# Kernel optimization log

Measured on AMD Instinct MI355X. Metric: run time of the kernel, lower is better.

The kernel has to match this reference:

```python
import math
import jax, jax.numpy as jnp
import numpy as np

B, S, D, H = 2, 2048, 1024, 16
DH = D // H
DFF = 4 * D
EPS = 1e-6
MASKED_BIAS = -10000.0


def _gelu(x):
    # GPT-2 tanh-approx GELU
    return 0.5 * x * (1.0 + jnp.tanh(math.sqrt(2.0 / math.pi) * (x + 0.044715 * x ** 3)))


def _layernorm(x, w, b):
    mean = jnp.mean(x, axis=-1, keepdims=True)
    var = jnp.mean((x - mean) ** 2, axis=-1, keepdims=True)
    return w * ((x - mean) / jnp.sqrt(var + EPS)) + b


def setup_inputs() -> dict:
    key = jax.random.key(0)
    ks = jax.random.split(key, 6)
    std = 0.02
    return {
        "hidden_states": jax.random.normal(ks[0], (B, S, D), jnp.float32),
        "w_attn": jax.random.normal(ks[1], (D, 3 * D), jnp.float32) * std,
        "b_attn": jnp.zeros((3 * D,), jnp.float32),
        "w_proj": jax.random.normal(ks[2], (D, D), jnp.float32) * std,
        "b_proj": jnp.zeros((D,), jnp.float32),
        "w_fc": jax.random.normal(ks[3], (D, DFF), jnp.float32) * std,
        "b_fc": jnp.zeros((DFF,), jnp.float32),
        "w_fc_proj": jax.random.normal(ks[4], (DFF, D), jnp.float32) * std,
        "b_fc_proj": jnp.zeros((D,), jnp.float32),
        "ln1_w": jnp.ones((D,), jnp.float32),
        "ln1_b": jnp.zeros((D,), jnp.float32),
        "ln2_w": jnp.ones((D,), jnp.float32),
        "ln2_b": jnp.zeros((D,), jnp.float32),
    }


def reference(hidden_states, w_attn, b_attn, w_proj, b_proj, w_fc, b_fc,
              w_fc_proj, b_fc_proj, ln1_w, ln1_b, ln2_w, ln2_b):
    residual = hidden_states
    x = _layernorm(hidden_states, ln1_w, ln1_b)

    # c_attn: [B,S,D] @ [D,3D] + b -> split into q,k,v
    qkv = x @ w_attn + b_attn
    q, k, v = jnp.split(qkv, 3, axis=-1)
    # split heads -> [B,H,S,DH]
    q = q.reshape(B, S, H, DH).transpose(0, 2, 1, 3)
    k = k.reshape(B, S, H, DH).transpose(0, 2, 1, 3)
    v = v.reshape(B, S, H, DH).transpose(0, 2, 1, 3)

    scores = jnp.einsum('bhqd,bhkd->bhqk', q, k) / jnp.sqrt(jnp.float32(DH))
    causal = jnp.tril(jnp.ones((S, S), bool))  # [S,S]
    scores = jnp.where(causal[None, None], scores, jnp.float32(MASKED_BIAS))
    attn = jax.nn.softmax(scores, axis=-1)
    out = jnp.einsum('bhqk,bhkd->bhqd', attn, v)
    out = out.transpose(0, 2, 1, 3).reshape(B, S, D)
    out = out @ w_proj + b_proj

    h = residual + out
    residual = h
    y = _layernorm(h, ln2_w, ln2_b)
    y = _gelu(y @ w_fc + b_fc)
    y = y @ w_fc_proj + b_fc_proj
    return residual + y
```

## Files before the change

kernel.cpp:

```cpp
#include <hip/hip_runtime.h>
#include <cstdint>
#include <cstddef>

typedef unsigned short u16;
typedef float  floatx4 __attribute__((ext_vector_type(4)));
typedef short  short8  __attribute__((ext_vector_type(8)));
typedef u16    usx4    __attribute__((ext_vector_type(4)));
typedef u16    usx8    __attribute__((ext_vector_type(8)));
typedef unsigned uintx2 __attribute__((ext_vector_type(2)));

__device__ __forceinline__ u16 f2b(float f) {
  unsigned u = __float_as_uint(f);
  unsigned r = u + 0x7fffu + ((u >> 16) & 1u);
  return (u16)(r >> 16);
}
__device__ __forceinline__ float b2f(u16 s) {
  return __uint_as_float(((unsigned)s) << 16);
}

__device__ __forceinline__ float gelu_f(float x) {
  const float k = 2.3022082f;
  float u = x * (1.0f + 0.044715f * x * x);
  float t = __builtin_amdgcn_exp2f(-k * u);
  return x * __builtin_amdgcn_rcpf(1.0f + t);
}

__device__ __forceinline__ void gl2lds16(const u16* g, u16* l) {
  __builtin_amdgcn_global_load_lds(
      (const __attribute__((address_space(1))) unsigned int*)g,
      (__attribute__((address_space(3))) unsigned int*)l, 16, 0, 0);
}

#define C2SCALE 0.18033688011112042f

__global__ __launch_bounds__(256) void ln_bf16_kernel(
    const float* __restrict__ in, const float* __restrict__ w,
    const float* __restrict__ b, u16* __restrict__ out)
{
  const int row = blockIdx.x;
  const int t = threadIdx.x;
  const float* p = in + (size_t)row * 1024 + t * 4;
  floatx4 v = *(const floatx4*)p;
  float s  = v.x + v.y + v.z + v.w;
  float ss = v.x*v.x + v.y*v.y + v.z*v.z + v.w*v.w;
  #pragma unroll
  for (int m = 1; m < 64; m <<= 1) {
    s  += __shfl_xor(s,  m);
    ss += __shfl_xor(ss, m);
  }
  __shared__ float red[8];
  if ((t & 63) == 0) { red[(t >> 6)*2] = s; red[(t >> 6)*2 + 1] = ss; }
  __syncthreads();
  s  = red[0] + red[2] + red[4] + red[6];
  ss = red[1] + red[3] + red[5] + red[7];
  const float mean = s * (1.0f / 1024.0f);
  const float var  = ss * (1.0f / 1024.0f) - mean * mean;
  const float rstd = rsqrtf(var + 1e-6f);
  floatx4 wv = *(const floatx4*)(w + t * 4);
  floatx4 bv = *(const floatx4*)(b + t * 4);
  usx4 o = { f2b(wv.x * ((v.x - mean) * rstd) + bv.x),
             f2b(wv.y * ((v.y - mean) * rstd) + bv.y),
             f2b(wv.z * ((v.z - mean) * rstd) + bv.z),
             f2b(wv.w * ((v.w - mean) * rstd) + bv.w) };
  *(usx4*)(out + (size_t)row * 1024 + t * 4) = o;
}

__global__ __launch_bounds__(256) void combine_ln_kernel(
    const u16* __restrict__ p0, const u16* __restrict__ p1,
    const float* __restrict__ res, const float* __restrict__ bias,
    const float* __restrict__ w, const float* __restrict__ b,
    float* __restrict__ hout, u16* __restrict__ yout)
{
  const int row = blockIdx.x;
  const int t = threadIdx.x;
  const size_t i0 = (size_t)row * 1024 + t * 4;
  floatx4 rv = *(const floatx4*)(res + i0);
  usx4 a = *(const usx4*)(p0 + i0);
  usx4 c = *(const usx4*)(p1 + i0);
  floatx4 biasv = *(const floatx4*)(bias + t * 4);
  floatx4 v;
  #pragma unroll
  for (int i = 0; i < 4; ++i) v[i] = rv[i] + b2f(a[i]) + b2f(c[i]) + biasv[i];
  *(floatx4*)(hout + i0) = v;

  float s  = v.x + v.y + v.z + v.w;
  float ss = v.x*v.x + v.y*v.y + v.z*v.z + v.w*v.w;
  #pragma unroll
  for (int m = 1; m < 64; m <<= 1) {
    s  += __shfl_xor(s,  m);
    ss += __shfl_xor(ss, m);
  }
  __shared__ float red[8];
  if ((t & 63) == 0) { red[(t >> 6)*2] = s; red[(t >> 6)*2 + 1] = ss; }
  __syncthreads();
  s  = red[0] + red[2] + red[4] + red[6];
  ss = red[1] + red[3] + red[5] + red[7];
  const float mean = s * (1.0f / 1024.0f);
  const float var  = ss * (1.0f / 1024.0f) - mean * mean;
  const float rstd = rsqrtf(var + 1e-6f);
  floatx4 wv = *(const floatx4*)(w + t * 4);
  floatx4 bv = *(const floatx4*)(b + t * 4);
  usx4 o = { f2b(wv.x * ((v.x - mean) * rstd) + bv.x),
             f2b(wv.y * ((v.y - mean) * rstd) + bv.y),
             f2b(wv.z * ((v.z - mean) * rstd) + bv.z),
             f2b(wv.w * ((v.w - mean) * rstd) + bv.w) };
  *(usx4*)(yout + i0) = o;
}

__device__ __forceinline__ void wtrans_body(
    const float* __restrict__ in, u16* __restrict__ out, int K, int N,
    int bx, int by, int tx, int ty)
{
  __shared__ u16 tile[32][33];
  const int n0 = bx * 32, k0 = by * 32;
  #pragma unroll
  for (int i = 0; i < 4; ++i)
    tile[ty + i*8][tx] = f2b(in[(size_t)(k0 + ty + i*8) * N + n0 + tx]);
  __syncthreads();
  #pragma unroll
  for (int i = 0; i < 4; ++i)
    out[(size_t)(n0 + ty + i*8) * K + k0 + tx] = tile[tx][ty + i*8];
}

__global__ __launch_bounds__(256) void wtrans4_kernel(
    const float* __restrict__ w0, const float* __restrict__ w1,
    const float* __restrict__ w2, const float* __restrict__ w3,
    u16* __restrict__ o0, u16* __restrict__ o1,
    u16* __restrict__ o2, u16* __restrict__ o3)
{
  int blk = blockIdx.x;
  const int tx = threadIdx.x & 31, ty = threadIdx.x >> 5;
  if (blk < 3072) {
    wtrans_body(w0, o0, 1024, 3072, blk % 96, blk / 96, tx, ty);
  } else if (blk < 4096) {
    blk -= 3072; wtrans_body(w1, o1, 1024, 1024, blk % 32, blk / 32, tx, ty);
  } else if (blk < 8192) {
    blk -= 4096; wtrans_body(w2, o2, 1024, 4096, blk % 128, blk / 128, tx, ty);
  } else {
    blk -= 8192; wtrans_body(w3, o3, 4096, 1024, blk % 32, blk / 32, tx, ty);
  }
}

template<int BM, int BN, int FLAGS, int MINW,
         int NX, int NY, int NZ, int RX, int RY, int RZ>
__global__ __launch_bounds__(256, MINW) void gemm_mfma_kernel(
    const u16* __restrict__ A, const u16* __restrict__ Bt,
    const float* __restrict__ bias, const float* __restrict__ Res,
    void* __restrict__ Cout, int M, int N, int K, int kLen, size_t zStride)
{
  constexpr int WM = BM / 2, WN = BN / 2;
  constexpr int MT = WM / 16, NT = WN / 16;
  constexpr int GX = NX / RX, GY = NY / RY, GZ = NZ / RZ;
  __shared__ u16 As[BM * 32];
  __shared__ u16 Bs[BN * 32];

  const int lin = blockIdx.x + NX * (blockIdx.y + NY * blockIdx.z);
  const int xcd = lin & 7;
  const int idx = lin >> 3;
  const int rx = xcd % RX, ry = (xcd / RX) % RY, rz = xcd / (RX * RY);
  const int bx = rx * GX + idx % GX;
  const int by = ry * GY + (idx / GX) % GY;
  const int bz = rz * GZ + idx / (GX * GY);

  const int t = threadIdx.x;
  const int wave = t >> 6, lane = t & 63;
  const int quad = lane >> 4, l16 = lane & 15;
  const int wm = wave >> 1, wn = wave & 1;
  const int bm0 = by * BM, bn0 = bx * BN;
  const int kStart = bz * kLen;

  const int sRow = lane >> 2;
  const int sq   = (lane & 3) ^ ((lane >> 4) & 3);

  const u16* aG[BM / 64];
  u16* aL[BM / 64];
  #pragma unroll
  for (int j = 0; j < BM / 64; ++j) {
    const int band = j * 4 + wave;
    aG[j] = A + (size_t)(bm0 + band * 16 + sRow) * K + kStart + sq * 8;
    aL[j] = As + band * 512;
  }
  const u16* bG[BN / 64];
  u16* bL[BN / 64];
  #pragma unroll
  for (int j = 0; j < BN / 64; ++j) {
    const int band = j * 4 + wave;
    bG[j] = Bt + (size_t)(bn0 + band * 16 + sRow) * K + kStart + sq * 8;
    bL[j] = Bs + band * 512;
  }

  floatx4 acc[MT][NT] = {};
  const int rcol = (quad ^ (l16 >> 2)) << 3;

  for (int k0 = 0; k0 < kLen; k0 += 32) {
    __syncthreads();
    #pragma unroll
    for (int j = 0; j < BM / 64; ++j) gl2lds16(aG[j] + k0, aL[j]);
    #pragma unroll
    for (int j = 0; j < BN / 64; ++j) gl2lds16(bG[j] + k0, bL[j]);
    __syncthreads();

    short8 af[MT], bf[NT];
    #pragma unroll
    for (int mt = 0; mt < MT; ++mt)
      af[mt] = *(const short8*)&As[(wm*WM + mt*16 + l16) * 32 + rcol];
    #pragma unroll
    for (int nt = 0; nt < NT; ++nt)
      bf[nt] = *(const short8*)&Bs[(wn*WN + nt*16 + l16) * 32 + rcol];
    #pragma unroll
    for (int mt = 0; mt < MT; ++mt)
      #pragma unroll
      for (int nt = 0; nt < NT; ++nt)
        acc[mt][nt] = __builtin_amdgcn_mfma_f32_16x16x32_bf16(af[mt], bf[nt], acc[mt][nt], 0, 0, 0);
  }

  const int orow0 = bm0 + wm * WM;
  const int ocol0 = bn0 + wn * WN;
  const size_t zoff = (size_t)bz * zStride;
  #pragma unroll
  for (int nt = 0; nt < NT; ++nt) {
    const int col = ocol0 + nt*16 + l16;
    const float bv = bias ? bias[col] : 0.0f;
    const float postscale = ((FLAGS & 8) && col < 1024) ? C2SCALE : 1.0f;
    #pragma unroll
    for (int mt = 0; mt < MT; ++mt) {
      #pragma unroll
      for (int r = 0; r < 4; ++r) {
        const int row = orow0 + mt*16 + quad*4 + r;
        float v = acc[mt][nt][r] + bv;
        if (FLAGS & 1) v = gelu_f(v);
        if (FLAGS & 8) v *= postscale;
        if (FLAGS & 2) v += Res[(size_t)row * N + col];
        if (FLAGS & 4) ((u16*)Cout)[zoff + (size_t)row * N + col] = f2b(v);
        else           ((float*)Cout)[zoff + (size_t)row * N + col] = v;
      }
    }
  }
}

__global__ __launch_bounds__(256, 4) void attn_mfma_kernel(
    const u16* __restrict__ qkv, u16* __restrict__ opart, float* __restrict__ ml)
{
  __shared__ u16 Ks[64][72];
  __shared__ u16 Vt[64][72];
  __shared__ u16 Ps[64][72];

  const int t    = threadIdx.x;
  const int wave = t >> 6;
  const int lane = t & 63;
  const int quad = lane >> 4;
  const int l16  = lane & 15;
  const int pair = blockIdx.x >> 1;
  const int half = blockIdx.x & 1;
  const int h    = blockIdx.y;
  const int b    = blockIdx.z;

  const size_t base = (size_t)b * 2048 * 3072;
  const int qoff = h * 64;
  const int koff = 1024 + h * 64;
  const int voff = 2048 + h * 64;

  const int prow = t >> 2;
  const int scol = (t & 3) * 16;
  const int kmap = ((prow & 15) << 2) | (prow >> 4);
  const int kpair  = t & 31;
  const int vchunk = t >> 5;

  const size_t obase  = ((((size_t)half * 2 + b) * 16 + h) * 2048) * 64;
  const size_t mlbase = ((((size_t)half * 2 + b) * 16 + h) * 2048) * 2;

  short8 onesb;
  {
    const short v = (l16 == 0) ? (short)0x3F80 : (short)0;
    #pragma unroll
    for (int i = 0; i < 8; ++i) onesb[i] = v;
  }

  #pragma unroll 1
  for (int iter = 0; iter < 2; ++iter) {
    const int qi = iter ? (31 - pair) : pair;
    const int q0 = qi << 6;
    const int T  = qi + 1;
    const int mid = (T + 1) >> 1;
    const int t0 = half ? mid : 0;
    const int t1 = half ? T : mid;

    floatx4 of[4] = {};
    floatx4 ofl = {};
    float m[4];
    #pragma unroll
    for (int r = 0; r < 4; ++r) m[r] = -1e30f;

    if (t0 < t1) {
      __syncthreads();
      {
        const u16* qp = qkv + base + (size_t)(q0 + prow) * 3072 + qoff + scol;
        *(usx8*)&Ks[prow][scol]     = *(const usx8*)qp;
        *(usx8*)&Ks[prow][scol + 8] = *(const usx8*)(qp + 8);
      }
      __syncthreads();
      const short8 qf0 = *(const short8*)&Ks[wave*16 + l16][quad*8];
      const short8 qf1 = *(const short8*)&Ks[wave*16 + l16][32 + quad*8];

      usx8 kr0, kr1, vr0, vr1;
      {
        const int k0 = t0 << 6;
        const u16* kp = qkv + base + (size_t)(k0 + kmap) * 3072 + koff + scol;
        kr0 = *(const usx8*)kp; kr1 = *(const usx8*)(kp + 8);
        const u16* vp = qkv + base + (size_t)(k0 + 2*kpair) * 3072 + voff + vchunk*8;
        vr0 = *(const usx8*)vp; vr1 = *(const usx8*)(vp + 3072);
      }

      for (int tIdx = t0; tIdx < t1; ++tIdx) {
        __syncthreads();
        *(usx8*)&Ks[prow][scol]     = kr0;
        *(usx8*)&Ks[prow][scol + 8] = kr1;
        #pragma unroll
        for (int i = 0; i < 8; ++i)
          *(unsigned*)&Vt[vchunk*8 + i][2*kpair] =
              (unsigned)vr0[i] | ((unsigned)vr1[i] << 16);
        __syncthreads();

        if (tIdx + 1 < t1) {
          const int kn = (tIdx + 1) << 6;
          const u16* kp = qkv + base + (size_t)(kn + kmap) * 3072 + koff + scol;
          kr0 = *(const usx8*)kp; kr1 = *(const usx8*)(kp + 8);
          const u16* vp = qkv + base + (size_t)(kn + 2*kpair) * 3072 + voff + vchunk*8;
          vr0 = *(const usx8*)vp; vr1 = *(const usx8*)(vp + 3072);
        }

        const int k0 = tIdx << 6;
        floatx4 sf[4];
        #pragma unroll
        for (int kt = 0; kt < 4; ++kt) {
          short8 kf0 = *(const short8*)&Ks[kt*16 + l16][quad*8];
          short8 kf1 = *(const short8*)&Ks[kt*16 + l16][32 + quad*8];
          floatx4 z = {};
          z      = __builtin_amdgcn_mfma_f32_16x16x32_bf16(qf0, kf0, z, 0, 0, 0);
          sf[kt] = __builtin_amdgcn_mfma_f32_16x16x32_bf16(qf1, kf1, z, 0, 0, 0);
        }

        const bool diag = (tIdx == qi);
        #pragma unroll
        for (int r = 0; r < 4; ++r) {
          float sv0 = sf[0][r], sv1 = sf[1][r], sv2 = sf[2][r], sv3 = sf[3][r];
          if (diag) {
            const int qrow = q0 + wave*16 + quad*4 + r;
            const int kbase = k0 + 4*l16;
            if (kbase     > qrow) sv0 = -1e30f;
            if (kbase + 1 > qrow) sv1 = -1e30f;
            if (kbase + 2 > qrow) sv2 = -1e30f;
            if (kbase + 3 > qrow) sv3 = -1e30f;
          }
          float mx = fmaxf(fmaxf(sv0, sv1), fmaxf(sv2, sv3));
          #pragma unroll
          for (int msk = 1; msk < 16; msk <<= 1) mx = fmaxf(mx, __shfl_xor(mx, msk, 16));
          const float nm = fmaxf(m[r], mx);
          const float alpha = __builtin_amdgcn_exp2f(m[r] - nm);
          m[r] = nm;
          const unsigned e0 = f2b(__builtin_amdgcn_exp2f(sv0 - nm));
          const unsigned e1 = f2b(__builtin_amdgcn_exp2f(sv1 - nm));
          const unsigned e2 = f2b(__builtin_amdgcn_exp2f(sv2 - nm));
          const unsigned e3 = f2b(__builtin_amdgcn_exp2f(sv3 - nm));
          uintx2 pw = { e0 | (e1 << 16), e2 | (e3 << 16) };
          *(uintx2*)&Ps[wave*16 + quad*4 + r][l16 * 4] = pw;
          #pragma unroll
          for (int dht = 0; dht < 4; ++dht) of[dht][r] *= alpha;
          ofl[r] *= alpha;
        }

        short8 pf0 = *(const short8*)&Ps[wave*16 + l16][quad*8];
        short8 pf1 = *(const short8*)&Ps[wave*16 + l16][32 + quad*8];
        #pragma unroll
        for (int dht = 0; dht < 4; ++dht) {
          short8 vf0 = *(const short8*)&Vt[dht*16 + l16][quad*8];
          short8 vf1 = *(const short8*)&Vt[dht*16 + l16][32 + quad*8];
          of[dht] = __builtin_amdgcn_mfma_f32_16x16x32_bf16(pf0, vf0, of[dht], 0, 0, 0);
          of[dht] = __builtin_amdgcn_mfma_f32_16x16x32_bf16(pf1, vf1, of[dht], 0, 0, 0);
        }
        ofl = __builtin_amdgcn_mfma_f32_16x16x32_bf16(pf0, onesb, ofl, 0, 0, 0);
        ofl = __builtin_amdgcn_mfma_f32_16x16x32_bf16(pf1, onesb, ofl, 0, 0, 0);
      }
    }

    #pragma unroll
    for (int r = 0; r < 4; ++r) {
      const int s = q0 + wave*16 + quad*4 + r;
      u16* orow = opart + obase + (size_t)s * 64;
      #pragma unroll
      for (int dht = 0; dht < 4; ++dht) orow[dht*16 + l16] = f2b(of[dht][r]);
      const float lr = __shfl(ofl[r], quad * 16);
      if (l16 == 0) { ml[mlbase + 2*s] = m[r]; ml[mlbase + 2*s + 1] = lr; }
    }
  }
}

__global__ __launch_bounds__(256) void attn_combine_kernel(
    const u16* __restrict__ opart, const float* __restrict__ ml,
    u16* __restrict__ out)
{
  const int t = threadIdx.x;
  const int s = blockIdx.x * 4 + (t >> 6);
  const int lane = t & 63;
  const int h = blockIdx.y, b = blockIdx.z;

  const size_t o0  = ((((size_t)0 * 2 + b) * 16 + h) * 2048 + s) * 64 + lane;
  const size_t o1  = ((((size_t)1 * 2 + b) * 16 + h) * 2048 + s) * 64 + lane;
  const size_t ml0 = ((((size_t)0 * 2 + b) * 16 + h) * 2048 + s) * 2;
  const size_t ml1 = ((((size_t)1 * 2 + b) * 16 + h) * 2048 + s) * 2;

  const float m0 = ml[ml0], l0 = ml[ml0 + 1];
  const float m1 = ml[ml1], l1 = ml[ml1 + 1];
  const float M  = fmaxf(m0, m1);
  const float w0 = __builtin_amdgcn_exp2f(m0 - M);
  const float w1 = __builtin_amdgcn_exp2f(m1 - M);
  const float L  = w0 * l0 + w1 * l1;
  const float o  = w0 * b2f(opart[o0]) + w1 * b2f(opart[o1]);
  out[((size_t)b * 2048 + s) * 1024 + h * 64 + lane] = f2b(o / L);
}

__global__ __launch_bounds__(256) void ksplit_combine_kernel(
    const u16* __restrict__ p0, const u16* __restrict__ p1,
    const float* __restrict__ res, const float* __restrict__ bias,
    float* __restrict__ out)
{
  const size_t i0 = ((size_t)blockIdx.x * 256 + threadIdx.x) * 8;
  usx8 a = *(const usx8*)(p0 + i0);
  usx8 c = *(const usx8*)(p1 + i0);
  const int col = (int)(i0 & 1023);
  floatx4 bv0 = *(const floatx4*)(bias + col);
  floatx4 bv1 = *(const floatx4*)(bias + col + 4);
  floatx4 h0 = *(const floatx4*)(res + i0);
  floatx4 h1 = *(const floatx4*)(res + i0 + 4);
  floatx4 o0, o1;
  #pragma unroll
  for (int i = 0; i < 4; ++i) o0[i] = h0[i] + b2f(a[i])   + b2f(c[i])   + bv0[i];
  #pragma unroll
  for (int i = 0; i < 4; ++i) o1[i] = h1[i] + b2f(a[4+i]) + b2f(c[4+i]) + bv1[i];
  *(floatx4*)(out + i0)     = o0;
  *(floatx4*)(out + i0 + 4) = o1;
}

extern "C" void kernel_launch(void* const* d_in, const int* in_sizes, int n_in,
                              void* d_out, int out_size, void* d_ws, size_t ws_size,
                              hipStream_t stream) {
  const float* hidden    = (const float*)d_in[0];
  const float* w_attn    = (const float*)d_in[1];
  const float* b_attn    = (const float*)d_in[2];
  const float* w_proj    = (const float*)d_in[3];
  const float* b_proj    = (const float*)d_in[4];
  const float* w_fc      = (const float*)d_in[5];
  const float* b_fc      = (const float*)d_in[6];
  const float* w_fc_proj = (const float*)d_in[7];
  const float* b_fc_proj = (const float*)d_in[8];
  const float* ln1_w     = (const float*)d_in[9];
  const float* ln1_b     = (const float*)d_in[10];
  const float* ln2_w     = (const float*)d_in[11];
  const float* ln2_b     = (const float*)d_in[12];

  char* wsb = (char*)d_ws;
  u16*   qkvb  = (u16*)  (wsb + (size_t)( 0u << 20));
  u16*   xb    = (u16*)  (wsb + (size_t)(24u << 20));
  u16*   opart = (u16*)  (wsb + (size_t)(24u << 20));
  float* mlbuf = (float*)(wsb + (size_t)(40u << 20));
  u16*   attnb = (u16*)  (wsb + (size_t)(42u << 20));
  u16*   wqT   = (u16*)  (wsb + (size_t)(50u << 20));
  u16*   wpT   = (u16*)  (wsb + (size_t)(56u << 20));
  u16*   wfT   = (u16*)  (wsb + (size_t)(58u << 20));
  u16*   wfpT  = (u16*)  (wsb + (size_t)(66u << 20));
  u16*   pproj = (u16*)  (wsb + (size_t)(24u << 20));
  float* hbuf  = (float*)(wsb + (size_t)(42u << 20));
  u16*   yb    = (u16*)  (wsb + (size_t)( 0u << 20));
  u16*   fcb   = (u16*)  (wsb + (size_t)( 8u << 20));
  u16*   pfcp0 = (u16*)  (wsb + (size_t)( 0u << 20));
  u16*   pfcp1 = (u16*)  (wsb + (size_t)(58u << 20));
  const size_t zstr_fcp = ((size_t)58u << 20) / 2;

  wtrans4_kernel<<<dim3(12288), 256, 0, stream>>>(
      w_attn, w_proj, w_fc, w_fc_proj, wqT, wpT, wfT, wfpT);

  ln_bf16_kernel<<<4096, 256, 0, stream>>>(hidden, ln1_w, ln1_b, xb);
  gemm_mfma_kernel<128,128,12,4, 24,32,1, 2,4,1><<<dim3(24, 32, 1), 256, 0, stream>>>(
      xb, wqT, b_attn, nullptr, qkvb, 4096, 3072, 1024, 1024, 0);
  attn_mfma_kernel<<<dim3(32, 16, 2), 256, 0, stream>>>(qkvb, opart, mlbuf);
  attn_combine_kernel<<<dim3(512, 16, 2), 256, 0, stream>>>(opart, mlbuf, attnb);
  gemm_mfma_kernel<128,64,4,4, 16,32,2, 1,4,2><<<dim3(16, 32, 2), 256, 0, stream>>>(
      attnb, wpT, nullptr, nullptr, pproj, 4096, 1024, 1024, 512, 4194304);
  combine_ln_kernel<<<4096, 256, 0, stream>>>(
      pproj, pproj + 4194304, hidden, b_proj, ln2_w, ln2_b, hbuf, yb);
  gemm_mfma_kernel<128,128,5,4, 32,32,1, 2,4,1><<<dim3(32, 32, 1), 256, 0, stream>>>(
      yb, wfT, b_fc, nullptr, fcb, 4096, 4096, 1024, 1024, 0);
  gemm_mfma_kernel<128,64,4,4, 16,32,2, 1,4,2><<<dim3(16, 32, 2), 256, 0, stream>>>(
      fcb, wfpT, nullptr, nullptr, pfcp0, 4096, 1024, 4096, 2048, zstr_fcp);
  ksplit_combine_kernel<<<dim3(2048), 256, 0, stream>>>(
      pfcp0, pfcp1, hbuf, b_fc_proj, (float*)d_out);
}
```

Before: 356.3 us.

## Double-buffer GEMM LDS tiles and use DPP row-max and packed bf16 conversion

The GEMM main loop now keeps two LDS buffers and issues the global-to-LDS loads for the next K slice before computing the current one, so load latency overlaps with MFMA work. In the attention kernel, the 16-lane max reduction uses DPP row operations instead of shuffles, and the manual bf16 rounding is replaced by the hardware v_cvt_pk_bf16_f32 instruction. The cost is doubled LDS use per GEMM block, which may lower occupancy. The unrolled-by-two loop also assumes kLen is a multiple of 64.

Measured after the change: 352.3 us. No clear change (-1.1%).

```diff
diff --git a/kernel.cpp b/kernel.cpp
--- a/kernel.cpp
+++ b/kernel.cpp
@@ -16,6 +16,25 @@
 }
 __device__ __forceinline__ float b2f(u16 s) {
   return __uint_as_float(((unsigned)s) << 16);
+}
+
+__device__ __forceinline__ unsigned cvt_pk_bf16(float lo, float hi) {
+  unsigned r;
+  asm("v_cvt_pk_bf16_f32 %0, %1, %2" : "=v"(r) : "v"(lo), "v"(hi));
+  return r;
+}
+
+__device__ __forceinline__ float rowmax16(float x) {
+  int xi = __float_as_int(x), y;
+  y = __builtin_amdgcn_update_dpp(xi, xi, 0xB1, 0xF, 0xF, false);
+  x = fmaxf(x, __int_as_float(y)); xi = __float_as_int(x);
+  y = __builtin_amdgcn_update_dpp(xi, xi, 0x4E, 0xF, 0xF, false);
+  x = fmaxf(x, __int_as_float(y)); xi = __float_as_int(x);
+  y = __builtin_amdgcn_update_dpp(xi, xi, 0x141, 0xF, 0xF, false);
+  x = fmaxf(x, __int_as_float(y)); xi = __float_as_int(x);
+  y = __builtin_amdgcn_update_dpp(xi, xi, 0x140, 0xF, 0xF, false);
+  x = fmaxf(x, __int_as_float(y));
+  return x;
 }
 
 __device__ __forceinline__ float gelu_f(float x) {
@@ -151,8 +170,8 @@
   constexpr int WM = BM / 2, WN = BN / 2;
   constexpr int MT = WM / 16, NT = WN / 16;
   constexpr int GX = NX / RX, GY = NY / RY, GZ = NZ / RZ;
-  __shared__ u16 As[BM * 32];
-  __shared__ u16 Bs[BN * 32];
+  __shared__ u16 As[2 * BM * 32];
+  __shared__ u16 Bs[2 * BN * 32];
 
   const int lin = blockIdx.x + NX * (blockIdx.y + NY * blockIdx.z);
   const int xcd = lin & 7;
@@ -192,26 +211,35 @@
   floatx4 acc[MT][NT] = {};
   const int rcol = (quad ^ (l16 >> 2)) << 3;
 
-  for (int k0 = 0; k0 < kLen; k0 += 32) {
-    __syncthreads();
-    #pragma unroll
-    for (int j = 0; j < BM / 64; ++j) gl2lds16(aG[j] + k0, aL[j]);
-    #pragma unroll
-    for (int j = 0; j < BN / 64; ++j) gl2lds16(bG[j] + k0, bL[j]);
-    __syncthreads();
-
+  auto stage = [&](int koff, int buf) {
+    #pragma unroll
+    for (int j = 0; j < BM / 64; ++j) gl2lds16(aG[j] + koff, aL[j] + buf * (BM * 32));
+    #pragma unroll
+    for (int j = 0; j < BN / 64; ++j) gl2lds16(bG[j] + koff, bL[j] + buf * (BN * 32));
+  };
+  auto compute = [&](const u16* Asc, const u16* Bsc) {
     short8 af[MT], bf[NT];
     #pragma unroll
     for (int mt = 0; mt < MT; ++mt)
-      af[mt] = *(const short8*)&As[(wm*WM + mt*16 + l16) * 32 + rcol];
+      af[mt] = *(const short8*)&Asc[(wm*WM + mt*16 + l16) * 32 + rcol];
     #pragma unroll
     for (int nt = 0; nt < NT; ++nt)
-      bf[nt] = *(const short8*)&Bs[(wn*WN + nt*16 + l16) * 32 + rcol];
+      bf[nt] = *(const short8*)&Bsc[(wn*WN + nt*16 + l16) * 32 + rcol];
     #pragma unroll
     for (int mt = 0; mt < MT; ++mt)
       #pragma unroll
       for (int nt = 0; nt < NT; ++nt)
         acc[mt][nt] = __builtin_amdgcn_mfma_f32_16x16x32_bf16(af[mt], bf[nt], acc[mt][nt], 0, 0, 0);
+  };
+
+  stage(0, 0);
+  for (int k0 = 0; k0 < kLen; k0 += 64) {
+    __syncthreads();
+    stage(k0 + 32, 1);
+    compute(As, Bs);
+    __syncthreads();
+    if (k0 + 64 < kLen) stage(k0 + 64, 0);
+    compute(As + BM * 32, Bs + BN * 32);
   }
 
   const int orow0 = bm0 + wm * WM;
@@ -353,16 +381,15 @@
             if (kbase + 3 > qrow) sv3 = -1e30f;
           }
           float mx = fmaxf(fmaxf(sv0, sv1), fmaxf(sv2, sv3));
-          #pragma unroll
-          for (int msk = 1; msk < 16; msk <<= 1) mx = fmaxf(mx, __shfl_xor(mx, msk, 16));
+          mx = rowmax16(mx);
           const float nm = fmaxf(m[r], mx);
           const float alpha = __builtin_amdgcn_exp2f(m[r] - nm);
           m[r] = nm;
-          const unsigned e0 = f2b(__builtin_amdgcn_exp2f(sv0 - nm));
-          const unsigned e1 = f2b(__builtin_amdgcn_exp2f(sv1 - nm));
-          const unsigned e2 = f2b(__builtin_amdgcn_exp2f(sv2 - nm));
-          const unsigned e3 = f2b(__builtin_amdgcn_exp2f(sv3 - nm));
-          uintx2 pw = { e0 | (e1 << 16), e2 | (e3 << 16) };
+          const float p0 = __builtin_amdgcn_exp2f(sv0 - nm);
+          const float p1 = __builtin_amdgcn_exp2f(sv1 - nm);
+          const float p2 = __builtin_amdgcn_exp2f(sv2 - nm);
+          const float p3 = __builtin_amdgcn_exp2f(sv3 - nm);
+          uintx2 pw = { cvt_pk_bf16(p0, p1), cvt_pk_bf16(p2, p3) };
           *(uintx2*)&Ps[wave*16 + quad*4 + r][l16 * 4] = pw;
           #pragma unroll
           for (int dht = 0; dht < 4; ++dht) of[dht][r] *= alpha;
```
